# Kernel tuning notes

Hardware: AMD Instinct MI355X
Metric: run time of the kernel (lower is better)

## Reference

```python
import jax, jax.numpy as jnp
import numpy as np

N, E, C_IN, H, K = 16384, 524288, 128, 64, 64


def setup_inputs() -> dict:
    key = jax.random.key(0)
    ks = jax.random.split(key, 6)
    x = jax.random.normal(ks[0], (N, C_IN), dtype=jnp.float32)
    edge_index = jax.random.randint(ks[1], (2, E), 0, N, dtype=jnp.int32)
    edge_weight = jax.random.uniform(ks[2], (E,), dtype=jnp.float32)
    sc = lambda f: 1.0 / np.sqrt(f)
    # GCNConv lin (no bias inside lin; separate bias), Glorot-ish init
    W1 = jax.random.normal(ks[3], (C_IN, H), dtype=jnp.float32) * sc(C_IN)
    b1 = jnp.zeros((H,), jnp.float32)
    # DMoNPooling MLP: Linear(H,H) then Linear(H,K), no activation between (act=None)
    Wm1 = jax.random.normal(ks[4], (H, H), dtype=jnp.float32) * sc(H)
    bm1 = jnp.zeros((H,), jnp.float32)
    Wm2 = jax.random.normal(ks[5], (H, K), dtype=jnp.float32) * sc(H)
    bm2 = jnp.zeros((K,), jnp.float32)
    return dict(x=x, edge_index=edge_index, edge_weight=edge_weight,
                W1=W1, b1=b1, Wm1=Wm1, bm1=bm1, Wm2=Wm2, bm2=bm2)


def gcn_conv(x, edge_index, edge_weight, W, b, n):
    # GCNConv: add self-loops (weight 1), symmetric deg^-1/2 normalization,
    # aggregate messages from source (row) into target (col).
    row, col = edge_index[0], edge_index[1]
    loop = jnp.arange(n, dtype=edge_index.dtype)
    row = jnp.concatenate([row, loop])
    col = jnp.concatenate([col, loop])
    w = jnp.concatenate([edge_weight, jnp.ones((n,), edge_weight.dtype)])
    deg = jax.ops.segment_sum(w, col, num_segments=n)
    dis = jnp.where(deg > 0, jax.lax.rsqrt(deg), 0.0)
    norm = dis[row] * w * dis[col]
    xw = x @ W  # [N, H]
    out = jax.ops.segment_sum(xw[row] * norm[:, None], col, num_segments=n)
    return out + b


def dmon_pool(h, adj, Wm1, bm1, Wm2, bm2):
    # eval mode: dropout disabled
    s = jax.nn.softmax((h @ Wm1 + bm1) @ Wm2 + bm2, axis=-1)  # [N, K]
    k = s.shape[-1]
    out_adj = s.T @ (adj @ s)  # [K, K]

    # Spectral (modularity) loss; degrees = einsum('ijk->ik', adj) = column sums
    deg = adj.sum(axis=0)  # [N]
    m = deg.sum() / 2
    ca = s.T @ deg  # [K], equals degrees^T s as well (symmetric roles)
    normalizer = jnp.outer(ca, ca) / 2 / m
    spectral_loss = -jnp.trace(out_adj - normalizer) / 2 / m

    # Orthogonality loss
    ss = s.T @ s  # [K, K]
    ss_fro = jnp.sqrt(jnp.sum(ss * ss))
    i_fro = jnp.sqrt(jnp.float32(k))  # ||I_K||_F
    diff = ss / ss_fro - jnp.eye(k, dtype=ss.dtype) / i_fro
    ortho_loss = jnp.sqrt(jnp.sum(diff * diff))

    # Cluster size loss
    cluster_size = s.sum(axis=0)  # [K]
    cluster_loss = jnp.sqrt(jnp.sum(cluster_size * cluster_size)) / h.shape[0] * i_fro - 1.0

    return s, spectral_loss, ortho_loss, cluster_loss


def reference(x, edge_index, edge_weight, W1, b1, Wm1, bm1, Wm2, bm2):
    h = jax.nn.relu(gcn_conv(x, edge_index, edge_weight, W1, b1, N))
    # to_dense_adj(edge_index): dense [N, N], duplicate edges summed
    adj = jnp.zeros((N, N), h.dtype).at[edge_index[0], edge_index[1]].add(1.0)
    s, spec, ortho, clus = dmon_pool(h, adj, Wm1, bm1, Wm2, bm2)
    return s[None], spec + ortho + clus
```

## Files before the change

### kernel.cpp

```cpp
#include <hip/hip_runtime.h>
#include <hip/hip_bf16.h>

typedef float          f4  __attribute__((ext_vector_type(4)));
typedef unsigned short us4 __attribute__((ext_vector_type(4)));
typedef int            i2  __attribute__((ext_vector_type(2)));

template <typename T>
__device__ __forceinline__ T ntload(const T* p) { return __builtin_nontemporal_load(p); }

__device__ __forceinline__ unsigned short f2bf(float f) {
    unsigned u = __float_as_uint(f);
    return (unsigned short)((u + 0x7FFF + ((u >> 16) & 1)) >> 16);
}
__device__ __forceinline__ float bf2f(unsigned short h) {
    return __uint_as_float((unsigned)h << 16);
}

__global__ __launch_bounds__(256) void k_degxw(const int* __restrict__ ei,
                      const float* __restrict__ ew,
                      unsigned long long* __restrict__ deg_rep,
                      const float* __restrict__ x, const float* __restrict__ W1,
                      float* __restrict__ xw, unsigned short* __restrict__ xw16,
                      int N, int E) {
    __shared__ float w1l[128 * 64];
    __shared__ f4    xt[16][32];
    if (blockIdx.x < 2048) {
        int e = blockIdx.x * 256 + threadIdx.x;
        if (e < E) {
            int c = ntload(ei + E + e);
            float w = ntload(ew + e);
            unsigned q = (unsigned)__float2uint_rn(w * 16777216.f);
            unsigned long long p = (1ULL << 40) | (unsigned long long)q;
            atomicAdd(&deg_rep[(size_t)(blockIdx.x & 7) * N + c], p);
        }
        return;
    }
    int xbid = blockIdx.x - 2048;
    for (int t = threadIdx.x; t < 128 * 64; t += 256) w1l[t] = W1[t];
    int lane = threadIdx.x & 63;
    int wv   = threadIdx.x >> 6;
    for (int base = xbid * 16; base < N; base += 512 * 16) {
        __syncthreads();
        for (int t = threadIdx.x; t < 16 * 32; t += 256)
            ((f4*)xt)[t] = ntload((const f4*)x + (size_t)base * 32 + t);
        __syncthreads();
        int r0 = wv * 4;
        float a0 = 0.f, a1 = 0.f, a2 = 0.f, a3 = 0.f;
#pragma unroll
        for (int q = 0; q < 32; ++q) {
            f4 x0 = xt[r0][q], x1 = xt[r0 + 1][q], x2 = xt[r0 + 2][q], x3 = xt[r0 + 3][q];
            float wa = w1l[(4 * q + 0) * 64 + lane];
            float wb = w1l[(4 * q + 1) * 64 + lane];
            float wc = w1l[(4 * q + 2) * 64 + lane];
            float wd = w1l[(4 * q + 3) * 64 + lane];
            a0 = fmaf(x0.x, wa, a0); a0 = fmaf(x0.y, wb, a0); a0 = fmaf(x0.z, wc, a0); a0 = fmaf(x0.w, wd, a0);
            a1 = fmaf(x1.x, wa, a1); a1 = fmaf(x1.y, wb, a1); a1 = fmaf(x1.z, wc, a1); a1 = fmaf(x1.w, wd, a1);
            a2 = fmaf(x2.x, wa, a2); a2 = fmaf(x2.y, wb, a2); a2 = fmaf(x2.z, wc, a2); a2 = fmaf(x2.w, wd, a2);
            a3 = fmaf(x3.x, wa, a3); a3 = fmaf(x3.y, wb, a3); a3 = fmaf(x3.z, wc, a3); a3 = fmaf(x3.w, wd, a3);
        }
        int gr = base + r0;
        __builtin_nontemporal_store(a0, xw + (size_t)(gr + 0) * 64 + lane);
        __builtin_nontemporal_store(a1, xw + (size_t)(gr + 1) * 64 + lane);
        __builtin_nontemporal_store(a2, xw + (size_t)(gr + 2) * 64 + lane);
        __builtin_nontemporal_store(a3, xw + (size_t)(gr + 3) * 64 + lane);
        xw16[(size_t)(gr + 0) * 64 + lane] = f2bf(a0);
        xw16[(size_t)(gr + 1) * 64 + lane] = f2bf(a1);
        xw16[(size_t)(gr + 2) * 64 + lane] = f2bf(a2);
        xw16[(size_t)(gr + 3) * 64 + lane] = f2bf(a3);
    }
}

__global__ void k_red(const unsigned long long* __restrict__ deg_rep,
                      int* __restrict__ off_rep, int* __restrict__ cnt,
                      float* __restrict__ dis, int N) {
    int c = blockIdx.x * blockDim.x + threadIdx.x;
    if (c >= N) return;
    int run = 0;
    unsigned long long wsum = 0;
#pragma unroll
    for (int rep = 0; rep < 8; ++rep) {
        unsigned long long p = deg_rep[(size_t)rep * N + c];
        off_rep[(size_t)rep * N + c] = run;
        run += (int)(p >> 40);
        wsum += (p & ((1ULL << 40) - 1));
    }
    cnt[c] = run;
    dis[c] = rsqrtf((float)wsum * (1.f / 16777216.f) + 1.0f);
}

__global__ void k_scan(const int* __restrict__ cnt, int* __restrict__ offs, int N) {
    __shared__ int part[1024];
    int tid = threadIdx.x;
    int C = (N + 1023) / 1024;
    int base = tid * C;
    int loc[16];
    int sum = 0;
#pragma unroll
    for (int i = 0; i < 16; ++i) {
        if (i < C) {
            int idx = base + i;
            loc[i] = sum;
            sum += (idx < N) ? cnt[idx] : 0;
        }
    }
    part[tid] = sum;
    __syncthreads();
    for (int o = 1; o < 1024; o <<= 1) {
        int t = (tid >= o) ? part[tid - o] : 0;
        __syncthreads();
        part[tid] += t;
        __syncthreads();
    }
    int excl = part[tid] - sum;
#pragma unroll
    for (int i = 0; i < 16; ++i) {
        if (i < C) {
            int idx = base + i;
            if (idx < N) offs[idx] = excl + loc[i];
        }
    }
    if (tid == 1023) offs[N] = part[tid];
}

__global__ void k_bucket(const int* __restrict__ ei, const float* __restrict__ ew,
                         const float* __restrict__ dis, const int* __restrict__ offs,
                         const int* __restrict__ off_rep, int* __restrict__ cursor_rep,
                         i2* __restrict__ barr, int N, int E) {
    int e = blockIdx.x * blockDim.x + threadIdx.x;
    if (e < E) {
        int rep = blockIdx.x & 7;
        int r = ntload(ei + e), c = ntload(ei + E + e);
        float norm = dis[r] * ntload(ew + e) * dis[c];
        size_t rc = (size_t)rep * N + c;
        int pos = offs[c] + off_rep[rc] + atomicAdd(&cursor_rep[rc], 1);
        i2 rec; rec.x = r; rec.y = __float_as_int(norm);
        __builtin_nontemporal_store(rec, barr + pos);
    }
}

__global__ __launch_bounds__(256) void k_gather(const int* __restrict__ offs,
                         const i2* __restrict__ barr,
                         const float* __restrict__ xw, const unsigned short* __restrict__ xw16,
                         const float* __restrict__ dis,
                         const float* __restrict__ b1, float* __restrict__ h, int N) {
    int lane = threadIdx.x & 63;
    int sub = lane >> 4, q = lane & 15;
    int wid  = blockIdx.x * 4 + (threadIdx.x >> 6);
    int nw   = 4 * gridDim.x;
    const us4* xw16v = (const us4*)xw16;
    for (int cp = wid; cp < (N >> 1); cp += nw) {
        int c0 = 2 * cp, c1 = c0 + 1;
        int beg = ntload(offs + c0), mid = ntload(offs + c1), end = ntload(offs + c1 + 1);
        f4 A0 = {0.f, 0.f, 0.f, 0.f}, A1 = A0, B0 = A0, B1 = A0;
        for (int i = beg; i < end; i += 64) {
            int nloc = min(64, end - i);
            bool ok = (i + lane < end);
            i2 b = ok ? ntload(barr + i + lane) : (i2){0, 0};
            int   rv = b.x;
            float nv = __int_as_float(b.y);
            int jmax = (nloc + 3) >> 2;
            int j = 0;
            for (; j + 4 <= jmax; j += 4) {
                int e0 = 4 * j + sub;
                int g0 = i + e0;
                int   r0 = __shfl(rv, e0),      r1 = __shfl(rv, e0 + 4);
                int   r2 = __shfl(rv, e0 + 8),  r3 = __shfl(rv, e0 + 12);
                float n0 = __shfl(nv, e0),      n1 = __shfl(nv, e0 + 4);
                float n2 = __shfl(nv, e0 + 8),  n3 = __shfl(nv, e0 + 12);
                us4 u0 = xw16v[(size_t)r0 * 16 + q];
                us4 u1 = xw16v[(size_t)r1 * 16 + q];
                us4 u2 = xw16v[(size_t)r2 * 16 + q];
                us4 u3 = xw16v[(size_t)r3 * 16 + q];
                float a0w = (g0      < mid) ? n0 : 0.f, b0w = n0 - a0w;
                float a1w = (g0 + 4  < mid) ? n1 : 0.f, b1w = n1 - a1w;
                float a2w = (g0 + 8  < mid) ? n2 : 0.f, b2w = n2 - a2w;
                float a3w = (g0 + 12 < mid) ? n3 : 0.f, b3w = n3 - a3w;
                A0.x = fmaf(bf2f(u0.x), a0w, A0.x); A0.y = fmaf(bf2f(u0.y), a0w, A0.y);
                A0.z = fmaf(bf2f(u0.z), a0w, A0.z); A0.w = fmaf(bf2f(u0.w), a0w, A0.w);
                B0.x = fmaf(bf2f(u0.x), b0w, B0.x); B0.y = fmaf(bf2f(u0.y), b0w, B0.y);
                B0.z = fmaf(bf2f(u0.z), b0w, B0.z); B0.w = fmaf(bf2f(u0.w), b0w, B0.w);
                A1.x = fmaf(bf2f(u1.x), a1w, A1.x); A1.y = fmaf(bf2f(u1.y), a1w, A1.y);
                A1.z = fmaf(bf2f(u1.z), a1w, A1.z); A1.w = fmaf(bf2f(u1.w), a1w, A1.w);
                B1.x = fmaf(bf2f(u1.x), b1w, B1.x); B1.y = fmaf(bf2f(u1.y), b1w, B1.y);
                B1.z = fmaf(bf2f(u1.z), b1w, B1.z); B1.w = fmaf(bf2f(u1.w), b1w, B1.w);
                A0.x = fmaf(bf2f(u2.x), a2w, A0.x); A0.y = fmaf(bf2f(u2.y), a2w, A0.y);
                A0.z = fmaf(bf2f(u2.z), a2w, A0.z); A0.w = fmaf(bf2f(u2.w), a2w, A0.w);
                B0.x = fmaf(bf2f(u2.x), b2w, B0.x); B0.y = fmaf(bf2f(u2.y), b2w, B0.y);
                B0.z = fmaf(bf2f(u2.z), b2w, B0.z); B0.w = fmaf(bf2f(u2.w), b2w, B0.w);
                A1.x = fmaf(bf2f(u3.x), a3w, A1.x); A1.y = fmaf(bf2f(u3.y), a3w, A1.y);
                A1.z = fmaf(bf2f(u3.z), a3w, A1.z); A1.w = fmaf(bf2f(u3.w), a3w, A1.w);
                B1.x = fmaf(bf2f(u3.x), b3w, B1.x); B1.y = fmaf(bf2f(u3.y), b3w, B1.y);
                B1.z = fmaf(bf2f(u3.z), b3w, B1.z); B1.w = fmaf(bf2f(u3.w), b3w, B1.w);
            }
            for (; j < jmax; ++j) {
                int e = 4 * j + sub;
                int g = i + e;
                int   r  = __shfl(rv, e);
                float nm = __shfl(nv, e);
                us4 u = xw16v[(size_t)r * 16 + q];
                float aw = (g < mid) ? nm : 0.f, bw = nm - aw;
                A0.x = fmaf(bf2f(u.x), aw, A0.x); A0.y = fmaf(bf2f(u.y), aw, A0.y);
                A0.z = fmaf(bf2f(u.z), aw, A0.z); A0.w = fmaf(bf2f(u.w), aw, A0.w);
                B0.x = fmaf(bf2f(u.x), bw, B0.x); B0.y = fmaf(bf2f(u.y), bw, B0.y);
                B0.z = fmaf(bf2f(u.z), bw, B0.z); B0.w = fmaf(bf2f(u.w), bw, B0.w);
            }
        }
        A0.x += A1.x; A0.y += A1.y; A0.z += A1.z; A0.w += A1.w;
        B0.x += B1.x; B0.y += B1.y; B0.z += B1.z; B0.w += B1.w;
        A0.x += __shfl_xor(A0.x, 16); A0.y += __shfl_xor(A0.y, 16);
        A0.z += __shfl_xor(A0.z, 16); A0.w += __shfl_xor(A0.w, 16);
        B0.x += __shfl_xor(B0.x, 16); B0.y += __shfl_xor(B0.y, 16);
        B0.z += __shfl_xor(B0.z, 16); B0.w += __shfl_xor(B0.w, 16);
        A0.x += __shfl_xor(A0.x, 32); A0.y += __shfl_xor(A0.y, 32);
        A0.z += __shfl_xor(A0.z, 32); A0.w += __shfl_xor(A0.w, 32);
        B0.x += __shfl_xor(B0.x, 32); B0.y += __shfl_xor(B0.y, 32);
        B0.z += __shfl_xor(B0.z, 32); B0.w += __shfl_xor(B0.w, 32);
        f4 bb = ((const f4*)b1)[q];
        f4 self0 = ntload((const f4*)xw + (size_t)c0 * 16 + q);
        f4 self1 = ntload((const f4*)xw + (size_t)c1 * 16 + q);
        float d0 = dis[c0], d1 = dis[c1];
        float dd0 = d0 * d0, dd1 = d1 * d1;
        f4 v0, v1;
        v0.x = A0.x + self0.x * dd0 + bb.x; v0.y = A0.y + self0.y * dd0 + bb.y;
        v0.z = A0.z + self0.z * dd0 + bb.z; v0.w = A0.w + self0.w * dd0 + bb.w;
        v1.x = B0.x + self1.x * dd1 + bb.x; v1.y = B0.y + self1.y * dd1 + bb.y;
        v1.z = B0.z + self1.z * dd1 + bb.z; v1.w = B0.w + self1.w * dd1 + bb.w;
        v0.x = v0.x > 0.f ? v0.x : 0.f; v0.y = v0.y > 0.f ? v0.y : 0.f;
        v0.z = v0.z > 0.f ? v0.z : 0.f; v0.w = v0.w > 0.f ? v0.w : 0.f;
        v1.x = v1.x > 0.f ? v1.x : 0.f; v1.y = v1.y > 0.f ? v1.y : 0.f;
        v1.z = v1.z > 0.f ? v1.z : 0.f; v1.w = v1.w > 0.f ? v1.w : 0.f;
        if (sub == 0) {
            __builtin_nontemporal_store(v0, (f4*)h + (size_t)c0 * 16 + q);
            __builtin_nontemporal_store(v1, (f4*)h + (size_t)c1 * 16 + q);
        }
    }
}

__global__ __launch_bounds__(256) void k_mlp(const float* __restrict__ h,
                      const float* __restrict__ Wm1, const float* __restrict__ bm1,
                      const float* __restrict__ Wm2, const float* __restrict__ bm2,
                      float* __restrict__ s, unsigned short* __restrict__ s16, int N) {
    __shared__ float w1l[4096], w2l[4096], b1l[64], b2l[64];
    __shared__ f4    ht[16][16];
    __shared__ float tt[4][4][64];
    for (int t = threadIdx.x; t < 4096; t += 256) {
        w1l[t] = Wm1[t];
        w2l[t] = Wm2[t];
    }
    if (threadIdx.x < 64) {
        b1l[threadIdx.x] = bm1[threadIdx.x];
        b2l[threadIdx.x] = bm2[threadIdx.x];
    }
    int lane = threadIdx.x & 63;
    int wv   = threadIdx.x >> 6;
    for (int base = blockIdx.x * 16; base < N; base += gridDim.x * 16) {
        __syncthreads();
        for (int t = threadIdx.x; t < 16 * 16; t += 256)
            ((f4*)ht)[t] = ntload((const f4*)h + (size_t)base * 16 + t);
        __syncthreads();
        int r0 = wv * 4;
        float t0 = b1l[lane], t1 = t0, t2 = t0, t3 = t0;
#pragma unroll
        for (int q = 0; q < 16; ++q) {
            f4 h0 = ht[r0][q], h1 = ht[r0 + 1][q], h2 = ht[r0 + 2][q], h3 = ht[r0 + 3][q];
            float wa = w1l[(4 * q + 0) * 64 + lane];
            float wb = w1l[(4 * q + 1) * 64 + lane];
            float wc = w1l[(4 * q + 2) * 64 + lane];
            float wd = w1l[(4 * q + 3) * 64 + lane];
            t0 = fmaf(h0.x, wa, t0); t0 = fmaf(h0.y, wb, t0); t0 = fmaf(h0.z, wc, t0); t0 = fmaf(h0.w, wd, t0);
            t1 = fmaf(h1.x, wa, t1); t1 = fmaf(h1.y, wb, t1); t1 = fmaf(h1.z, wc, t1); t1 = fmaf(h1.w, wd, t1);
            t2 = fmaf(h2.x, wa, t2); t2 = fmaf(h2.y, wb, t2); t2 = fmaf(h2.z, wc, t2); t2 = fmaf(h2.w, wd, t2);
            t3 = fmaf(h3.x, wa, t3); t3 = fmaf(h3.y, wb, t3); t3 = fmaf(h3.z, wc, t3); t3 = fmaf(h3.w, wd, t3);
        }
        tt[wv][0][lane] = t0; tt[wv][1][lane] = t1;
        tt[wv][2][lane] = t2; tt[wv][3][lane] = t3;
        __syncthreads();
        float g0 = b2l[lane], g1 = g0, g2 = g0, g3 = g0;
#pragma unroll
        for (int q = 0; q < 16; ++q) {
            f4 u0 = ((f4*)tt[wv][0])[q], u1 = ((f4*)tt[wv][1])[q];
            f4 u2 = ((f4*)tt[wv][2])[q], u3 = ((f4*)tt[wv][3])[q];
            float wa = w2l[(4 * q + 0) * 64 + lane];
            float wb = w2l[(4 * q + 1) * 64 + lane];
            float wc = w2l[(4 * q + 2) * 64 + lane];
            float wd = w2l[(4 * q + 3) * 64 + lane];
            g0 = fmaf(u0.x, wa, g0); g0 = fmaf(u0.y, wb, g0); g0 = fmaf(u0.z, wc, g0); g0 = fmaf(u0.w, wd, g0);
            g1 = fmaf(u1.x, wa, g1); g1 = fmaf(u1.y, wb, g1); g1 = fmaf(u1.z, wc, g1); g1 = fmaf(u1.w, wd, g1);
            g2 = fmaf(u2.x, wa, g2); g2 = fmaf(u2.y, wb, g2); g2 = fmaf(u2.z, wc, g2); g2 = fmaf(u2.w, wd, g2);
            g3 = fmaf(u3.x, wa, g3); g3 = fmaf(u3.y, wb, g3); g3 = fmaf(u3.z, wc, g3); g3 = fmaf(u3.w, wd, g3);
        }
        float m0 = g0, m1 = g1, m2 = g2, m3 = g3;
#pragma unroll
        for (int o = 32; o > 0; o >>= 1) {
            m0 = fmaxf(m0, __shfl_xor(m0, o));
            m1 = fmaxf(m1, __shfl_xor(m1, o));
            m2 = fmaxf(m2, __shfl_xor(m2, o));
            m3 = fmaxf(m3, __shfl_xor(m3, o));
        }
        float e0 = __expf(g0 - m0), e1 = __expf(g1 - m1);
        float e2 = __expf(g2 - m2), e3 = __expf(g3 - m3);
        float s0 = e0, s1 = e1, s2 = e2, s3 = e3;
#pragma unroll
        for (int o = 32; o > 0; o >>= 1) {
            s0 += __shfl_xor(s0, o);
            s1 += __shfl_xor(s1, o);
            s2 += __shfl_xor(s2, o);
            s3 += __shfl_xor(s3, o);
        }
        int gr = base + r0;
        float o0 = e0 / s0, o1 = e1 / s1, o2 = e2 / s2, o3 = e3 / s3;
        __builtin_nontemporal_store(o0, s + (size_t)(gr + 0) * 64 + lane);
        __builtin_nontemporal_store(o1, s + (size_t)(gr + 1) * 64 + lane);
        __builtin_nontemporal_store(o2, s + (size_t)(gr + 2) * 64 + lane);
        __builtin_nontemporal_store(o3, s + (size_t)(gr + 3) * 64 + lane);
        s16[(size_t)(gr + 0) * 64 + lane] = f2bf(o0);
        s16[(size_t)(gr + 1) * 64 + lane] = f2bf(o1);
        s16[(size_t)(gr + 2) * 64 + lane] = f2bf(o2);
        s16[(size_t)(gr + 3) * 64 + lane] = f2bf(o3);
    }
}

__global__ __launch_bounds__(256) void k_rt(const int* __restrict__ offs,
                         const i2* __restrict__ barr,
                         const unsigned short* __restrict__ s16,
                         const float* __restrict__ s, const int* __restrict__ cnt,
                         float* __restrict__ ssg, float* __restrict__ cag,
                         float* __restrict__ csg, float* __restrict__ tracearr, int N) {
    __shared__ float tile[64][64];
    __shared__ float bsum;
    int lane = threadIdx.x & 63;
    int wv   = threadIdx.x >> 6;
    if (blockIdx.x >= 2048) {
        int base = (blockIdx.x - 2048) * 64;
        if (base >= N) return;
        for (int t = threadIdx.x; t < 1024; t += 256)
            ((f4*)tile)[t] = ntload((const f4*)(s + (size_t)base * 64) + t);
        __syncthreads();
        float acc[16];
#pragma unroll
        for (int i = 0; i < 16; ++i) acc[i] = 0.f;
        for (int r = 0; r < 64; ++r) {
            float sj = tile[r][lane];
            const float* brow = &tile[r][wv * 16];
#pragma unroll
            for (int i = 0; i < 16; ++i) acc[i] = fmaf(brow[i], sj, acc[i]);
        }
        float csj = 0.f, caj = 0.f;
#pragma unroll
        for (int i = 0; i < 16; ++i) {
            int r = wv * 16 + i;
            float sj = tile[r][lane];
            csj += sj;
            caj = fmaf(sj, (float)cnt[base + r], caj);
        }
#pragma unroll
        for (int i = 0; i < 16; ++i) atomicAdd(&ssg[(wv * 16 + i) * 64 + lane], acc[i]);
        atomicAdd(&csg[lane], csj);
        atomicAdd(&cag[lane], caj);
        return;
    }
    int sub = lane >> 4, q = lane & 15;
    int wid  = blockIdx.x * 4 + wv;
    int nw   = 4 * 2048;
    const us4* s16v = (const us4*)s16;
    float tacc = 0.f;
    for (int cp = wid; cp < (N >> 1); cp += nw) {
        int c0 = 2 * cp, c1 = c0 + 1;
        int beg = ntload(offs + c0), mid = ntload(offs + c1), end = ntload(offs + c1 + 1);
        us4 scu0 = s16v[(size_t)c0 * 16 + q];
        us4 scu1 = s16v[(size_t)c1 * 16 + q];
        f4 sc0 = {bf2f(scu0.x), bf2f(scu0.y), bf2f(scu0.z), bf2f(scu0.w)};
        f4 sc1 = {bf2f(scu1.x), bf2f(scu1.y), bf2f(scu1.z), bf2f(scu1.w)};
        f4 A0 = {0.f, 0.f, 0.f, 0.f}, A1 = A0, B0 = A0, B1 = A0;
        for (int i = beg; i < end; i += 64) {
            int nloc = min(64, end - i);
            int rv = (i + lane < end) ? ntload(barr + i + lane).x : 0;
            int jmax = (nloc + 3) >> 2;
            int j = 0;
            for (; j + 4 <= jmax; j += 4) {
                int e0 = 4 * j + sub;
                int g0 = i + e0;
                int r0 = __shfl(rv, e0),     r1 = __shfl(rv, e0 + 4);
                int r2 = __shfl(rv, e0 + 8), r3 = __shfl(rv, e0 + 12);
                float n0 = (e0      < nloc) ? 1.f : 0.f;
                float n1 = (e0 + 4  < nloc) ? 1.f : 0.f;
                float n2 = (e0 + 8  < nloc) ? 1.f : 0.f;
                float n3 = (e0 + 12 < nloc) ? 1.f : 0.f;
                us4 u0 = s16v[(size_t)r0 * 16 + q];
                us4 u1 = s16v[(size_t)r1 * 16 + q];
                us4 u2 = s16v[(size_t)r2 * 16 + q];
                us4 u3 = s16v[(size_t)r3 * 16 + q];
                float a0w = (g0      < mid) ? n0 : 0.f, b0w = n0 - a0w;
                float a1w = (g0 + 4  < mid) ? n1 : 0.f, b1w = n1 - a1w;
                float a2w = (g0 + 8  < mid) ? n2 : 0.f, b2w = n2 - a2w;
                float a3w = (g0 + 12 < mid) ? n3 : 0.f, b3w = n3 - a3w;
                A0.x = fmaf(bf2f(u0.x), a0w, A0.x); A0.y = fmaf(bf2f(u0.y), a0w, A0.y);
                A0.z = fmaf(bf2f(u0.z), a0w, A0.z); A0.w = fmaf(bf2f(u0.w), a0w, A0.w);
                B0.x = fmaf(bf2f(u0.x), b0w, B0.x); B0.y = fmaf(bf2f(u0.y), b0w, B0.y);
                B0.z = fmaf(bf2f(u0.z), b0w, B0.z); B0.w = fmaf(bf2f(u0.w), b0w, B0.w);
                A1.x = fmaf(bf2f(u1.x), a1w, A1.x); A1.y = fmaf(bf2f(u1.y), a1w, A1.y);
                A1.z = fmaf(bf2f(u1.z), a1w, A1.z); A1.w = fmaf(bf2f(u1.w), a1w, A1.w);
                B1.x = fmaf(bf2f(u1.x), b1w, B1.x); B1.y = fmaf(bf2f(u1.y), b1w, B1.y);
                B1.z = fmaf(bf2f(u1.z), b1w, B1.z); B1.w = fmaf(bf2f(u1.w), b1w, B1.w);
                A0.x = fmaf(bf2f(u2.x), a2w, A0.x); A0.y = fmaf(bf2f(u2.y), a2w, A0.y);
                A0.z = fmaf(bf2f(u2.z), a2w, A0.z); A0.w = fmaf(bf2f(u2.w), a2w, A0.w);
                B0.x = fmaf(bf2f(u2.x), b2w, B0.x); B0.y = fmaf(bf2f(u2.y), b2w, B0.y);
                B0.z = fmaf(bf2f(u2.z), b2w, B0.z); B0.w = fmaf(bf2f(u2.w), b2w, B0.w);
                A1.x = fmaf(bf2f(u3.x), a3w, A1.x); A1.y = fmaf(bf2f(u3.y), a3w, A1.y);
                A1.z = fmaf(bf2f(u3.z), a3w, A1.z); A1.w = fmaf(bf2f(u3.w), a3w, A1.w);
                B1.x = fmaf(bf2f(u3.x), b3w, B1.x); B1.y = fmaf(bf2f(u3.y), b3w, B1.y);
                B1.z = fmaf(bf2f(u3.z), b3w, B1.z); B1.w = fmaf(bf2f(u3.w), b3w, B1.w);
            }
            for (; j < jmax; ++j) {
                int e = 4 * j + sub;
                int g = i + e;
                int r = __shfl(rv, e);
                float m = (e < nloc) ? 1.f : 0.f;
                us4 u = s16v[(size_t)r * 16 + q];
                float aw = (g < mid) ? m : 0.f, bw = m - aw;
                A0.x = fmaf(bf2f(u.x), aw, A0.x); A0.y = fmaf(bf2f(u.y), aw, A0.y);
                A0.z = fmaf(bf2f(u.z), aw, A0.z); A0.w = fmaf(bf2f(u.w), aw, A0.w);
                B0.x = fmaf(bf2f(u.x), bw, B0.x); B0.y = fmaf(bf2f(u.y), bw, B0.y);
                B0.z = fmaf(bf2f(u.z), bw, B0.z); B0.w = fmaf(bf2f(u.w), bw, B0.w);
            }
        }
        A0.x += A1.x; A0.y += A1.y; A0.z += A1.z; A0.w += A1.w;
        B0.x += B1.x; B0.y += B1.y; B0.z += B1.z; B0.w += B1.w;
        A0.x += __shfl_xor(A0.x, 16); A0.y += __shfl_xor(A0.y, 16);
        A0.z += __shfl_xor(A0.z, 16); A0.w += __shfl_xor(A0.w, 16);
        B0.x += __shfl_xor(B0.x, 16); B0.y += __shfl_xor(B0.y, 16);
        B0.z += __shfl_xor(B0.z, 16); B0.w += __shfl_xor(B0.w, 16);
        A0.x += __shfl_xor(A0.x, 32); A0.y += __shfl_xor(A0.y, 32);
        A0.z += __shfl_xor(A0.z, 32); A0.w += __shfl_xor(A0.w, 32);
        B0.x += __shfl_xor(B0.x, 32); B0.y += __shfl_xor(B0.y, 32);
        B0.z += __shfl_xor(B0.z, 32); B0.w += __shfl_xor(B0.w, 32);
        tacc += A0.x * sc0.x + A0.y * sc0.y + A0.z * sc0.z + A0.w * sc0.w;
        tacc += B0.x * sc1.x + B0.y * sc1.y + B0.z * sc1.z + B0.w * sc1.w;
    }
    tacc *= 0.25f;
#pragma unroll
    for (int o = 32; o > 0; o >>= 1) tacc += __shfl_xor(tacc, o);
    if (threadIdx.x == 0) bsum = 0.f;
    __syncthreads();
    if (lane == 0) atomicAdd(&bsum, tacc);
    __syncthreads();
    if (threadIdx.x == 0) tracearr[blockIdx.x] = bsum;
}

__global__ void k_final(const float* __restrict__ ssg, const float* __restrict__ cag,
                        const float* __restrict__ csg, const float* __restrict__ tracearr,
                        int ntr, float Ef, float Nf, float* __restrict__ out) {
    __shared__ float red[256];
    int tid = threadIdx.x;

    float a = 0.f;
    for (int t = tid; t < ntr; t += 256) a += tracearr[t];
    red[tid] = a; __syncthreads();
    for (int o = 128; o > 0; o >>= 1) { if (tid < o) red[tid] += red[tid + o]; __syncthreads(); }
    float trace = red[0]; __syncthreads();

    a = 0.f;
    for (int t = tid; t < 4096; t += 256) { float v = ssg[t]; a += v * v; }
    red[tid] = a; __syncthreads();
    for (int o = 128; o > 0; o >>= 1) { if (tid < o) red[tid] += red[tid + o]; __syncthreads(); }
    float ss_sumsq = red[0]; __syncthreads();

    a = (tid < 64) ? ssg[tid * 64 + tid] : 0.f;
    red[tid] = a; __syncthreads();
    for (int o = 128; o > 0; o >>= 1) { if (tid < o) red[tid] += red[tid + o]; __syncthreads(); }
    float tr_ss = red[0]; __syncthreads();

    a = (tid < 64) ? cag[tid] * cag[tid] : 0.f;
    red[tid] = a; __syncthreads();
    for (int o = 128; o > 0; o >>= 1) { if (tid < o) red[tid] += red[tid + o]; __syncthreads(); }
    float ca_ss = red[0]; __syncthreads();

    a = (tid < 64) ? csg[tid] * csg[tid] : 0.f;
    red[tid] = a; __syncthreads();
    for (int o = 128; o > 0; o >>= 1) { if (tid < o) red[tid] += red[tid + o]; __syncthreads(); }
    float cs_ss = red[0];

    if (tid == 0) {
        float spec = -(trace - ca_ss / Ef) / Ef;
        float ss_fro = sqrtf(ss_sumsq);
        float ortho = sqrtf(fmaxf(2.f - tr_ss / (4.f * ss_fro), 0.f));
        float clus = sqrtf(cs_ss) / Nf * 8.f - 1.f;
        out[0] = spec + ortho + clus;
    }
}

extern "C" void kernel_launch(void* const* d_in, const int* in_sizes, int n_in,
                              void* d_out, int out_size, void* d_ws, size_t ws_size,
                              hipStream_t stream) {
    const float* x   = (const float*)d_in[0];
    const int*   ei  = (const int*)d_in[1];
    const float* ew  = (const float*)d_in[2];
    const float* W1  = (const float*)d_in[3];
    const float* b1  = (const float*)d_in[4];
    const float* Wm1 = (const float*)d_in[5];
    const float* bm1 = (const float*)d_in[6];
    const float* Wm2 = (const float*)d_in[7];
    const float* bm2 = (const float*)d_in[8];
    float* out = (float*)d_out;

    const int N = in_sizes[0] / 128;
    const int E = in_sizes[2];
    const int TGRID = 2304;

    char* base = (char*)d_ws;
    unsigned long long* deg_rep = (unsigned long long*)base;
    int*   cursor_rep = (int*)(base + (size_t)64 * N);
    float* ssg = (float*)(base + (size_t)96 * N);
    float* cag = ssg + 4096;
    float* csg = cag + 64;
    size_t zbytes = (size_t)96 * N + (4096 + 128) * 4;
    char* up = base + ((zbytes + 15) & ~(size_t)15);
    int*   cnt = (int*)up;            up += (size_t)4 * N;
    float* dis = (float*)up;          up += (size_t)4 * N;
    int*   offs = (int*)up;           up += (size_t)4 * (N + 1);
    float* tracearr = (float*)up;     up += (size_t)4 * TGRID;
    up = (char*)(((size_t)up + 15) & ~(size_t)15);
    float* xw = (float*)up;           up += (size_t)4 * N * 64;
    float* h  = (float*)up;           up += (size_t)4 * N * 64;
    int*   off_rep = (int*)h;
    i2*    barr = (i2*)up;            up += (size_t)8 * E;
    unsigned short* xw16 = (unsigned short*)up; up += (size_t)2 * N * 64;
    unsigned short* s16  = (unsigned short*)up;
    float* sbuf = out;

    hipMemsetAsync(d_ws, 0, zbytes, stream);

    k_degxw<<<2560, 256, 0, stream>>>(ei, ew, deg_rep, x, W1, xw, xw16, N, E);
    k_red<<<(N + 255) / 256, 256, 0, stream>>>(deg_rep, off_rep, cnt, dis, N);
    k_scan<<<1, 1024, 0, stream>>>(cnt, offs, N);
    k_bucket<<<(E + 255) / 256, 256, 0, stream>>>(ei, ew, dis, offs, off_rep, cursor_rep, barr, N, E);
    k_gather<<<2048, 256, 0, stream>>>(offs, barr, xw, xw16, dis, b1, h, N);
    k_mlp<<<512, 256, 0, stream>>>(h, Wm1, bm1, Wm2, bm2, sbuf, s16, N);
    k_rt<<<TGRID, 256, 0, stream>>>(offs, barr, s16, sbuf, cnt, ssg, cag, csg, tracearr, N);
    k_final<<<1, 256, 0, stream>>>(ssg, cag, csg, tracearr, TGRID, (float)E, (float)N,
                                   out + (size_t)N * 64);
}
```

Before: 233.7 us.

## Fuse GCN gather with MLP softmax and fold final loss reduction into last block

The gather kernel now runs the two-layer MLP and softmax directly on each wave's freshly aggregated node rows. Weights sit in shared memory and the h values are broadcast with shuffles, so the intermediate h buffer and its write and read round trip go away. The separate final loss kernel is merged into the trace kernel using a done counter, so the last block to finish computes the loss. This removes two launches and one full N×64 memory pass, at the cost of a larger 512-thread block with 32KB of shared weights that may reduce occupancy in the gather.

```diff
diff --git a/kernel.cpp b/kernel.cpp
--- a/kernel.cpp
+++ b/kernel.cpp
@@ -138,15 +138,22 @@
     }
 }
 
-__global__ __launch_bounds__(256) void k_gather(const int* __restrict__ offs,
+__global__ __launch_bounds__(512) void k_gmlp(const int* __restrict__ offs,
                          const i2* __restrict__ barr,
                          const float* __restrict__ xw, const unsigned short* __restrict__ xw16,
-                         const float* __restrict__ dis,
-                         const float* __restrict__ b1, float* __restrict__ h, int N) {
+                         const float* __restrict__ dis, const float* __restrict__ b1,
+                         const float* __restrict__ Wm1, const float* __restrict__ bm1,
+                         const float* __restrict__ Wm2, const float* __restrict__ bm2,
+                         float* __restrict__ s, unsigned short* __restrict__ s16, int N) {
+    __shared__ float w1m[4096], w2m[4096];
+    __shared__ float tsc[8][2][64];
+    for (int t = threadIdx.x; t < 4096; t += 512) { w1m[t] = Wm1[t]; w2m[t] = Wm2[t]; }
+    __syncthreads();
     int lane = threadIdx.x & 63;
     int sub = lane >> 4, q = lane & 15;
-    int wid  = blockIdx.x * 4 + (threadIdx.x >> 6);
-    int nw   = 4 * gridDim.x;
+    int wv   = threadIdx.x >> 6;
+    int wid  = blockIdx.x * 8 + wv;
+    int nw   = 8 * gridDim.x;
     const us4* xw16v = (const us4*)xw16;
     for (int cp = wid; cp < (N >> 1); cp += nw) {
         int c0 = 2 * cp, c1 = c0 + 1;
@@ -229,232 +236,195 @@
         v0.z = v0.z > 0.f ? v0.z : 0.f; v0.w = v0.w > 0.f ? v0.w : 0.f;
         v1.x = v1.x > 0.f ? v1.x : 0.f; v1.y = v1.y > 0.f ? v1.y : 0.f;
         v1.z = v1.z > 0.f ? v1.z : 0.f; v1.w = v1.w > 0.f ? v1.w : 0.f;
-        if (sub == 0) {
-            __builtin_nontemporal_store(v0, (f4*)h + (size_t)c0 * 16 + q);
-            __builtin_nontemporal_store(v1, (f4*)h + (size_t)c1 * 16 + q);
-        }
-    }
-}
-
-__global__ __launch_bounds__(256) void k_mlp(const float* __restrict__ h,
-                      const float* __restrict__ Wm1, const float* __restrict__ bm1,
-                      const float* __restrict__ Wm2, const float* __restrict__ bm2,
-                      float* __restrict__ s, unsigned short* __restrict__ s16, int N) {
-    __shared__ float w1l[4096], w2l[4096], b1l[64], b2l[64];
-    __shared__ f4    ht[16][16];
-    __shared__ float tt[4][4][64];
-    for (int t = threadIdx.x; t < 4096; t += 256) {
-        w1l[t] = Wm1[t];
-        w2l[t] = Wm2[t];
-    }
-    if (threadIdx.x < 64) {
-        b1l[threadIdx.x] = bm1[threadIdx.x];
-        b2l[threadIdx.x] = bm2[threadIdx.x];
-    }
-    int lane = threadIdx.x & 63;
-    int wv   = threadIdx.x >> 6;
-    for (int base = blockIdx.x * 16; base < N; base += gridDim.x * 16) {
-        __syncthreads();
-        for (int t = threadIdx.x; t < 16 * 16; t += 256)
-            ((f4*)ht)[t] = ntload((const f4*)h + (size_t)base * 16 + t);
-        __syncthreads();
-        int r0 = wv * 4;
-        float t0 = b1l[lane], t1 = t0, t2 = t0, t3 = t0;
-#pragma unroll
-        for (int q = 0; q < 16; ++q) {
-            f4 h0 = ht[r0][q], h1 = ht[r0 + 1][q], h2 = ht[r0 + 2][q], h3 = ht[r0 + 3][q];
-            float wa = w1l[(4 * q + 0) * 64 + lane];
-            float wb = w1l[(4 * q + 1) * 64 + lane];
-            float wc = w1l[(4 * q + 2) * 64 + lane];
-            float wd = w1l[(4 * q + 3) * 64 + lane];
-            t0 = fmaf(h0.x, wa, t0); t0 = fmaf(h0.y, wb, t0); t0 = fmaf(h0.z, wc, t0); t0 = fmaf(h0.w, wd, t0);
-            t1 = fmaf(h1.x, wa, t1); t1 = fmaf(h1.y, wb, t1); t1 = fmaf(h1.z, wc, t1); t1 = fmaf(h1.w, wd, t1);
-            t2 = fmaf(h2.x, wa, t2); t2 = fmaf(h2.y, wb, t2); t2 = fmaf(h2.z, wc, t2); t2 = fmaf(h2.w, wd, t2);
-            t3 = fmaf(h3.x, wa, t3); t3 = fmaf(h3.y, wb, t3); t3 = fmaf(h3.z, wc, t3); t3 = fmaf(h3.w, wd, t3);
-        }
-        tt[wv][0][lane] = t0; tt[wv][1][lane] = t1;
-        tt[wv][2][lane] = t2; tt[wv][3][lane] = t3;
-        __syncthreads();
-        float g0 = b2l[lane], g1 = g0, g2 = g0, g3 = g0;
-#pragma unroll
-        for (int q = 0; q < 16; ++q) {
-            f4 u0 = ((f4*)tt[wv][0])[q], u1 = ((f4*)tt[wv][1])[q];
-            f4 u2 = ((f4*)tt[wv][2])[q], u3 = ((f4*)tt[wv][3])[q];
-            float wa = w2l[(4 * q + 0) * 64 + lane];
-            float wb = w2l[(4 * q + 1) * 64 + lane];
-            float wc = w2l[(4 * q + 2) * 64 + lane];
-            float wd = w2l[(4 * q + 3) * 64 + lane];
-            g0 = fmaf(u0.x, wa, g0); g0 = fmaf(u0.y, wb, g0); g0 = fmaf(u0.z, wc, g0); g0 = fmaf(u0.w, wd, g0);
-            g1 = fmaf(u1.x, wa, g1); g1 = fmaf(u1.y, wb, g1); g1 = fmaf(u1.z, wc, g1); g1 = fmaf(u1.w, wd, g1);
-            g2 = fmaf(u2.x, wa, g2); g2 = fmaf(u2.y, wb, g2); g2 = fmaf(u2.z, wc, g2); g2 = fmaf(u2.w, wd, g2);
-            g3 = fmaf(u3.x, wa, g3); g3 = fmaf(u3.y, wb, g3); g3 = fmaf(u3.z, wc, g3); g3 = fmaf(u3.w, wd, g3);
-        }
-        float m0 = g0, m1 = g1, m2 = g2, m3 = g3;
+        float t0 = bm1[lane], t1 = t0;
+#pragma unroll
+        for (int k = 0; k < 16; ++k) {
+            float wa = w1m[(4 * k + 0) * 64 + lane];
+            float wb = w1m[(4 * k + 1) * 64 + lane];
+            float wc = w1m[(4 * k + 2) * 64 + lane];
+            float wd = w1m[(4 * k + 3) * 64 + lane];
+            t0 = fmaf(__shfl(v0.x, k), wa, t0); t0 = fmaf(__shfl(v0.y, k), wb, t0);
+            t0 = fmaf(__shfl(v0.z, k), wc, t0); t0 = fmaf(__shfl(v0.w, k), wd, t0);
+            t1 = fmaf(__shfl(v1.x, k), wa, t1); t1 = fmaf(__shfl(v1.y, k), wb, t1);
+            t1 = fmaf(__shfl(v1.z, k), wc, t1); t1 = fmaf(__shfl(v1.w, k), wd, t1);
+        }
+        tsc[wv][0][lane] = t0;
+        tsc[wv][1][lane] = t1;
+        float g0 = bm2[lane], g1 = g0;
+#pragma unroll
+        for (int k = 0; k < 16; ++k) {
+            f4 ta = ((f4*)tsc[wv][0])[k];
+            f4 tb = ((f4*)tsc[wv][1])[k];
+            float wa = w2m[(4 * k + 0) * 64 + lane];
+            float wb = w2m[(4 * k + 1) * 64 + lane];
+            float wc = w2m[(4 * k + 2) * 64 + lane];
+            float wd = w2m[(4 * k + 3) * 64 + lane];
+            g0 = fmaf(ta.x, wa, g0); g0 = fmaf(ta.y, wb, g0);
+            g0 = fmaf(ta.z, wc, g0); g0 = fmaf(ta.w, wd, g0);
+            g1 = fmaf(tb.x, wa, g1); g1 = fmaf(tb.y, wb, g1);
+            g1 = fmaf(tb.z, wc, g1); g1 = fmaf(tb.w, wd, g1);
+        }
+        float m0 = g0, m1 = g1;
 #pragma unroll
         for (int o = 32; o > 0; o >>= 1) {
             m0 = fmaxf(m0, __shfl_xor(m0, o));
             m1 = fmaxf(m1, __shfl_xor(m1, o));
-            m2 = fmaxf(m2, __shfl_xor(m2, o));
-            m3 = fmaxf(m3, __shfl_xor(m3, o));
         }
         float e0 = __expf(g0 - m0), e1 = __expf(g1 - m1);
-        float e2 = __expf(g2 - m2), e3 = __expf(g3 - m3);
-        float s0 = e0, s1 = e1, s2 = e2, s3 = e3;
+        float z0 = e0, z1 = e1;
 #pragma unroll
         for (int o = 32; o > 0; o >>= 1) {
-            s0 += __shfl_xor(s0, o);
-            s1 += __shfl_xor(s1, o);
-            s2 += __shfl_xor(s2, o);
-            s3 += __shfl_xor(s3, o);
-        }
-        int gr = base + r0;
-        float o0 = e0 / s0, o1 = e1 / s1, o2 = e2 / s2, o3 = e3 / s3;
-        __builtin_nontemporal_store(o0, s + (size_t)(gr + 0) * 64 + lane);
-        __builtin_nontemporal_store(o1, s + (size_t)(gr + 1) * 64 + lane);
-        __builtin_nontemporal_store(o2, s + (size_t)(gr + 2) * 64 + lane);
-        __builtin_nontemporal_store(o3, s + (size_t)(gr + 3) * 64 + lane);
-        s16[(size_t)(gr + 0) * 64 + lane] = f2bf(o0);
-        s16[(size_t)(gr + 1) * 64 + lane] = f2bf(o1);
-        s16[(size_t)(gr + 2) * 64 + lane] = f2bf(o2);
-        s16[(size_t)(gr + 3) * 64 + lane] = f2bf(o3);
-    }
-}
-
-__global__ __launch_bounds__(256) void k_rt(const int* __restrict__ offs,
+            z0 += __shfl_xor(z0, o);
+            z1 += __shfl_xor(z1, o);
+        }
+        float o0 = e0 / z0, o1 = e1 / z1;
+        __builtin_nontemporal_store(o0, s + (size_t)c0 * 64 + lane);
+        __builtin_nontemporal_store(o1, s + (size_t)c1 * 64 + lane);
+        s16[(size_t)c0 * 64 + lane] = f2bf(o0);
+        s16[(size_t)c1 * 64 + lane] = f2bf(o1);
+    }
+}
+
+__global__ __launch_bounds__(256) void k_rtfin(const int* __restrict__ offs,
                          const i2* __restrict__ barr,
                          const unsigned short* __restrict__ s16,
                          const float* __restrict__ s, const int* __restrict__ cnt,
                          float* __restrict__ ssg, float* __restrict__ cag,
-                         float* __restrict__ csg, float* __restrict__ tracearr, int N) {
+                         float* __restrict__ csg, float* __restrict__ tracearr,
+                         unsigned* __restrict__ done, float Ef, float Nf,
+                         float* __restrict__ loss, int N) {
     __shared__ float tile[64][64];
     __shared__ float bsum;
+    __shared__ unsigned tck;
     int lane = threadIdx.x & 63;
     int wv   = threadIdx.x >> 6;
     if (blockIdx.x >= 2048) {
         int base = (blockIdx.x - 2048) * 64;
-        if (base >= N) return;
-        for (int t = threadIdx.x; t < 1024; t += 256)
-            ((f4*)tile)[t] = ntload((const f4*)(s + (size_t)base * 64) + t);
+        if (base < N) {
+            for (int t = threadIdx.x; t < 1024; t += 256)
+                ((f4*)tile)[t] = ntload((const f4*)(s + (size_t)base * 64) + t);
+            __syncthreads();
+            float acc[16];
+#pragma unroll
+            for (int i = 0; i < 16; ++i) acc[i] = 0.f;
+            for (int r = 0; r < 64; ++r) {
+                float sj = tile[r][lane];
+                const float* brow = &tile[r][wv * 16];
+#pragma unroll
+                for (int i = 0; i < 16; ++i) acc[i] = fmaf(brow[i], sj, acc[i]);
+            }
+            float csj = 0.f, caj = 0.f;
+#pragma unroll
+            for (int i = 0; i < 16; ++i) {
+                int r = wv * 16 + i;
+                float sj = tile[r][lane];
+                csj += sj;
+                caj = fmaf(sj, (float)cnt[base + r], caj);
+            }
+#pragma unroll
+            for (int i = 0; i < 16; ++i) atomicAdd(&ssg[(wv * 16 + i) * 64 + lane], acc[i]);
+            atomicAdd(&csg[lane], csj);
+            atomicAdd(&cag[lane], caj);
+        }
+    } else {
+        int sub = lane >> 4, q = lane & 15;
+        int wid  = blockIdx.x * 4 + wv;
+        int nw   = 4 * 2048;
+        const us4* s16v = (const us4*)s16;
+        float tacc = 0.f;
+        for (int cp = wid; cp < (N >> 1); cp += nw) {
+            int c0 = 2 * cp, c1 = c0 + 1;
+            int beg = ntload(offs + c0), mid = ntload(offs + c1), end = ntload(offs + c1 + 1);
+            us4 scu0 = s16v[(size_t)c0 * 16 + q];
+            us4 scu1 = s16v[(size_t)c1 * 16 + q];
+            f4 sc0 = {bf2f(scu0.x), bf2f(scu0.y), bf2f(scu0.z), bf2f(scu0.w)};
+            f4 sc1 = {bf2f(scu1.x), bf2f(scu1.y), bf2f(scu1.z), bf2f(scu1.w)};
+            f4 A0 = {0.f, 0.f, 0.f, 0.f}, A1 = A0, B0 = A0, B1 = A0;
+            for (int i = beg; i < end; i += 64) {
+                int nloc = min(64, end - i);
+                int rv = (i + lane < end) ? ntload(barr + i + lane).x : 0;
+                int jmax = (nloc + 3) >> 2;
+                int j = 0;
+                for (; j + 4 <= jmax; j += 4) {
+                    int e0 = 4 * j + sub;
+                    int g0 = i + e0;
+                    int r0 = __shfl(rv, e0),     r1 = __shfl(rv, e0 + 4);
+                    int r2 = __shfl(rv, e0 + 8), r3 = __shfl(rv, e0 + 12);
+                    float n0 = (e0      < nloc) ? 1.f : 0.f;
+                    float n1 = (e0 + 4  < nloc) ? 1.f : 0.f;
+                    float n2 = (e0 + 8  < nloc) ? 1.f : 0.f;
+                    float n3 = (e0 + 12 < nloc) ? 1.f : 0.f;
+                    us4 u0 = s16v[(size_t)r0 * 16 + q];
+                    us4 u1 = s16v[(size_t)r1 * 16 + q];
+                    us4 u2 = s16v[(size_t)r2 * 16 + q];
+                    us4 u3 = s16v[(size_t)r3 * 16 + q];
+                    float a0w = (g0      < mid) ? n0 : 0.f, b0w = n0 - a0w;
+                    float a1w = (g0 + 4  < mid) ? n1 : 0.f, b1w = n1 - a1w;
+                    float a2w = (g0 + 8  < mid) ? n2 : 0.f, b2w = n2 - a2w;
+                    float a3w = (g0 + 12 < mid) ? n3 : 0.f, b3w = n3 - a3w;
+                    A0.x = fmaf(bf2f(u0.x), a0w, A0.x); A0.y = fmaf(bf2f(u0.y), a0w, A0.y);
+                    A0.z = fmaf(bf2f(u0.z), a0w, A0.z); A0.w = fmaf(bf2f(u0.w), a0w, A0.w);
+                    B0.x = fmaf(bf2f(u0.x), b0w, B0.x); B0.y = fmaf(bf2f(u0.y), b0w, B0.y);
+                    B0.z = fmaf(bf2f(u0.z), b0w, B0.z); B0.w = fmaf(bf2f(u0.w), b0w, B0.w);
+                    A1.x = fmaf(bf2f(u1.x), a1w, A1.x); A1.y = fmaf(bf2f(u1.y), a1w, A1.y);
+                    A1.z = fmaf(bf2f(u1.z), a1w, A1.z); A1.w = fmaf(bf2f(u1.w), a1w, A1.w);
+                    B1.x = fmaf(bf2f(u1.x), b1w, B1.x); B1.y = fmaf(bf2f(u1.y), b1w, B1.y);
+                    B1.z = fmaf(bf2f(u1.z), b1w, B1.z); B1.w = fmaf(bf2f(u1.w), b1w, B1.w);
+                    A0.x = fmaf(bf2f(u2.x), a2w, A0.x); A0.y = fmaf(bf2f(u2.y), a2w, A0.y);
+                    A0.z = fmaf(bf2f(u2.z), a2w, A0.z); A0.w = fmaf(bf2f(u2.w), a2w, A0.w);
+                    B0.x = fmaf(bf2f(u2.x), b2w, B0.x); B0.y = fmaf(bf2f(u2.y), b2w, B0.y);
+                    B0.z = fmaf(bf2f(u2.z), b2w, B0.z); B0.w = fmaf(bf2f(u2.w), b2w, B0.w);
+                    A1.x = fmaf(bf2f(u3.x), a3w, A1.x); A1.y = fmaf(bf2f(u3.y), a3w, A1.y);
+                    A1.z = fmaf(bf2f(u3.z), a3w, A1.z); A1.w = fmaf(bf2f(u3.w), a3w, A1.w);
+                    B1.x = fmaf(bf2f(u3.x), b3w, B1.x); B1.y = fmaf(bf2f(u3.y), b3w, B1.y);
+                    B1.z = fmaf(bf2f(u3.z), b3w, B1.z); B1.w = fmaf(bf2f(u3.w), b3w, B1.w);
+                }
+                for (; j < jmax; ++j) {
+                    int e = 4 * j + sub;
+                    int g = i + e;
+                    int r = __shfl(rv, e);
+                    float m = (e < nloc) ? 1.f : 0.f;
+                    us4 u = s16v[(size_t)r * 16 + q];
+                    float aw = (g < mid) ? m : 0.f, bw = m - aw;
+                    A0.x = fmaf(bf2f(u.x), aw, A0.x); A0.y = fmaf(bf2f(u.y), aw, A0.y);
+                    A0.z = fmaf(bf2f(u.z), aw, A0.z); A0.w = fmaf(bf2f(u.w), aw, A0.w);
+                    B0.x = fmaf(bf2f(u.x), bw, B0.x); B0.y = fmaf(bf2f(u.y), bw, B0.y);
+                    B0.z = fmaf(bf2f(u.z), bw, B0.z); B0.w = fmaf(bf2f(u.w), bw, B0.w);
+                }
+            }
+            A0.x += A1.x; A0.y += A1.y; A0.z += A1.z; A0.w += A1.w;
+            B0.x += B1.x; B0.y += B1.y; B0.z += B1.z; B0.w += B1.w;
+            A0.x += __shfl_xor(A0.x, 16); A0.y += __shfl_xor(A0.y, 16);
+            A0.z += __shfl_xor(A0.z, 16); A0.w += __shfl_xor(A0.w, 16);
+            B0.x += __shfl_xor(B0.x, 16); B0.y += __shfl_xor(B0.y, 16);
+            B0.z += __shfl_xor(B0.z, 16); B0.w += __shfl_xor(B0.w, 16);
+            A0.x += __shfl_xor(A0.x, 32); A0.y += __shfl_xor(A0.y, 32);
+            A0.z += __shfl_xor(A0.z, 32); A0.w += __shfl_xor(A0.w, 32);
+            B0.x += __shfl_xor(B0.x, 32); B0.y += __shfl_xor(B0.y, 32);
+            B0.z += __shfl_xor(B0.z, 32); B0.w += __shfl_xor(B0.w, 32);
+            tacc += A0.x * sc0.x + A0.y * sc0.y + A0.z * sc0.z + A0.w * sc0.w;
+            tacc += B0.x * sc1.x + B0.y * sc1.y + B0.z * sc1.z + B0.w * sc1.w;
+        }
+        tacc *= 0.25f;
+#pragma unroll
+        for (int o = 32; o > 0; o >>= 1) tacc += __shfl_xor(tacc, o);
+        if (threadIdx.x == 0) bsum = 0.f;
         __syncthreads();
-        float acc[16];
-#pragma unroll
-        for (int i = 0; i < 16; ++i) acc[i] = 0.f;
-        for (int r = 0; r < 64; ++r) {
-            float sj = tile[r][lane];
-            const float* brow = &tile[r][wv * 16];
-#pragma unroll
-            for (int i = 0; i < 16; ++i) acc[i] = fmaf(brow[i], sj, acc[i]);
-        }
-        float csj = 0.f, caj = 0.f;
-#pragma unroll
-        for (int i = 0; i < 16; ++i) {
-            int r = wv * 16 + i;
-            float sj = tile[r][lane];
-            csj += sj;
-            caj = fmaf(sj, (float)cnt[base + r], caj);
-        }
-#pragma unroll
-        for (int i = 0; i < 16; ++i) atomicAdd(&ssg[(wv * 16 + i) * 64 + lane], acc[i]);
-        atomicAdd(&csg[lane], csj);
-        atomicAdd(&cag[lane], caj);
-        return;
-    }
-    int sub = lane >> 4, q = lane & 15;
-    int wid  = blockIdx.x * 4 + wv;
-    int nw   = 4 * 2048;
-    const us4* s16v = (const us4*)s16;
-    float tacc = 0.f;
-    for (int cp = wid; cp < (N >> 1); cp += nw) {
-        int c0 = 2 * cp, c1 = c0 + 1;
-        int beg = ntload(offs + c0), mid = ntload(offs + c1), end = ntload(offs + c1 + 1);
-        us4 scu0 = s16v[(size_t)c0 * 16 + q];
-        us4 scu1 = s16v[(size_t)c1 * 16 + q];
-        f4 sc0 = {bf2f(scu0.x), bf2f(scu0.y), bf2f(scu0.z), bf2f(scu0.w)};
-        f4 sc1 = {bf2f(scu1.x), bf2f(scu1.y), bf2f(scu1.z), bf2f(scu1.w)};
-        f4 A0 = {0.f, 0.f, 0.f, 0.f}, A1 = A0, B0 = A0, B1 = A0;
-        for (int i = beg; i < end; i += 64) {
-            int nloc = min(64, end - i);
-            int rv = (i + lane < end) ? ntload(barr + i + lane).x : 0;
-            int jmax = (nloc + 3) >> 2;
-            int j = 0;
-            for (; j + 4 <= jmax; j += 4) {
-                int e0 = 4 * j + sub;
-                int g0 = i + e0;
-                int r0 = __shfl(rv, e0),     r1 = __shfl(rv, e0 + 4);
-                int r2 = __shfl(rv, e0 + 8), r3 = __shfl(rv, e0 + 12);
-                float n0 = (e0      < nloc) ? 1.f : 0.f;
-                float n1 = (e0 + 4  < nloc) ? 1.f : 0.f;
-                float n2 = (e0 + 8  < nloc) ? 1.f : 0.f;
-                float n3 = (e0 + 12 < nloc) ? 1.f : 0.f;
-                us4 u0 = s16v[(size_t)r0 * 16 + q];
-                us4 u1 = s16v[(size_t)r1 * 16 + q];
-                us4 u2 = s16v[(size_t)r2 * 16 + q];
-                us4 u3 = s16v[(size_t)r3 * 16 + q];
-                float a0w = (g0      < mid) ? n0 : 0.f, b0w = n0 - a0w;
-                float a1w = (g0 + 4  < mid) ? n1 : 0.f, b1w = n1 - a1w;
-                float a2w = (g0 + 8  < mid) ? n2 : 0.f, b2w = n2 - a2w;
-                float a3w = (g0 + 12 < mid) ? n3 : 0.f, b3w = n3 - a3w;
-                A0.x = fmaf(bf2f(u0.x), a0w, A0.x); A0.y = fmaf(bf2f(u0.y), a0w, A0.y);
-                A0.z = fmaf(bf2f(u0.z), a0w, A0.z); A0.w = fmaf(bf2f(u0.w), a0w, A0.w);
-                B0.x = fmaf(bf2f(u0.x), b0w, B0.x); B0.y = fmaf(bf2f(u0.y), b0w, B0.y);
-                B0.z = fmaf(bf2f(u0.z), b0w, B0.z); B0.w = fmaf(bf2f(u0.w), b0w, B0.w);
-                A1.x = fmaf(bf2f(u1.x), a1w, A1.x); A1.y = fmaf(bf2f(u1.y), a1w, A1.y);
-                A1.z = fmaf(bf2f(u1.z), a1w, A1.z); A1.w = fmaf(bf2f(u1.w), a1w, A1.w);
-                B1.x = fmaf(bf2f(u1.x), b1w, B1.x); B1.y = fmaf(bf2f(u1.y), b1w, B1.y);
-                B1.z = fmaf(bf2f(u1.z), b1w, B1.z); B1.w = fmaf(bf2f(u1.w), b1w, B1.w);
-                A0.x = fmaf(bf2f(u2.x), a2w, A0.x); A0.y = fmaf(bf2f(u2.y), a2w, A0.y);
-                A0.z = fmaf(bf2f(u2.z), a2w, A0.z); A0.w = fmaf(bf2f(u2.w), a2w, A0.w);
-                B0.x = fmaf(bf2f(u2.x), b2w, B0.x); B0.y = fmaf(bf2f(u2.y), b2w, B0.y);
-                B0.z = fmaf(bf2f(u2.z), b2w, B0.z); B0.w = fmaf(bf2f(u2.w), b2w, B0.w);
-                A1.x = fmaf(bf2f(u3.x), a3w, A1.x); A1.y = fmaf(bf2f(u3.y), a3w, A1.y);
-                A1.z = fmaf(bf2f(u3.z), a3w, A1.z); A1.w = fmaf(bf2f(u3.w), a3w, A1.w);
-                B1.x = fmaf(bf2f(u3.x), b3w, B1.x); B1.y = fmaf(bf2f(u3.y), b3w, B1.y);
-                B1.z = fmaf(bf2f(u3.z), b3w, B1.z); B1.w = fmaf(bf2f(u3.w), b3w, B1.w);
-            }
-            for (; j < jmax; ++j) {
-                int e = 4 * j + sub;
-                int g = i + e;
-                int r = __shfl(rv, e);
-                float m = (e < nloc) ? 1.f : 0.f;
-                us4 u = s16v[(size_t)r * 16 + q];
-                float aw = (g < mid) ? m : 0.f, bw = m - aw;
-                A0.x = fmaf(bf2f(u.x), aw, A0.x); A0.y = fmaf(bf2f(u.y), aw, A0.y);
-                A0.z = fmaf(bf2f(u.z), aw, A0.z); A0.w = fmaf(bf2f(u.w), aw, A0.w);
-                B0.x = fmaf(bf2f(u.x), bw, B0.x); B0.y = fmaf(bf2f(u.y), bw, B0.y);
-                B0.z = fmaf(bf2f(u.z), bw, B0.z); B0.w = fmaf(bf2f(u.w), bw, B0.w);
-            }
-        }
-        A0.x += A1.x; A0.y += A1.y; A0.z += A1.z; A0.w += A1.w;
-        B0.x += B1.x; B0.y += B1.y; B0.z += B1.z; B0.w += B1.w;
-        A0.x += __shfl_xor(A0.x, 16); A0.y += __shfl_xor(A0.y, 16);
-        A0.z += __shfl_xor(A0.z, 16); A0.w += __shfl_xor(A0.w, 16);
-        B0.x += __shfl_xor(B0.x, 16); B0.y += __shfl_xor(B0.y, 16);
-        B0.z += __shfl_xor(B0.z, 16); B0.w += __shfl_xor(B0.w, 16);
-        A0.x += __shfl_xor(A0.x, 32); A0.y += __shfl_xor(A0.y, 32);
-        A0.z += __shfl_xor(A0.z, 32); A0.w += __shfl_xor(A0.w, 32);
-        B0.x += __shfl_xor(B0.x, 32); B0.y += __shfl_xor(B0.y, 32);
-        B0.z += __shfl_xor(B0.z, 32); B0.w += __shfl_xor(B0.w, 32);
-        tacc += A0.x * sc0.x + A0.y * sc0.y + A0.z * sc0.z + A0.w * sc0.w;
-        tacc += B0.x * sc1.x + B0.y * sc1.y + B0.z * sc1.z + B0.w * sc1.w;
-    }
-    tacc *= 0.25f;
-#pragma unroll
-    for (int o = 32; o > 0; o >>= 1) tacc += __shfl_xor(tacc, o);
-    if (threadIdx.x == 0) bsum = 0.f;
+        if (lane == 0) atomicAdd(&bsum, tacc);
+        __syncthreads();
+        if (threadIdx.x == 0) tracearr[blockIdx.x] = bsum;
+    }
     __syncthreads();
-    if (lane == 0) atomicAdd(&bsum, tacc);
+    __threadfence();
+    if (threadIdx.x == 0) tck = atomicAdd(done, 1u);
     __syncthreads();
-    if (threadIdx.x == 0) tracearr[blockIdx.x] = bsum;
-}
-
-__global__ void k_final(const float* __restrict__ ssg, const float* __restrict__ cag,
-                        const float* __restrict__ csg, const float* __restrict__ tracearr,
-                        int ntr, float Ef, float Nf, float* __restrict__ out) {
-    __shared__ float red[256];
+    if (tck != gridDim.x - 1u) return;
+    __threadfence();
+    float* red = &tile[0][0];
     int tid = threadIdx.x;
 
     float a = 0.f;
-    for (int t = tid; t < ntr; t += 256) a += tracearr[t];
+    for (int t = tid; t < 2048; t += 256) a += tracearr[t];
     red[tid] = a; __syncthreads();
     for (int o = 128; o > 0; o >>= 1) { if (tid < o) red[tid] += red[tid + o]; __syncthreads(); }
     float trace = red[0]; __syncthreads();
@@ -485,7 +455,7 @@
         float ss_fro = sqrtf(ss_sumsq);
         float ortho = sqrtf(fmaxf(2.f - tr_ss / (4.f * ss_fro), 0.f));
         float clus = sqrtf(cs_ss) / Nf * 8.f - 1.f;
-        out[0] = spec + ortho + clus;
+        loss[0] = spec + ortho + clus;
     }
 }
 
@@ -501,7 +471,6 @@
     const float* bm1 = (const float*)d_in[6];
     const float* Wm2 = (const float*)d_in[7];
     const float* bm2 = (const float*)d_in[8];
-    float* out = (float*)d_out;
 
     const int N = in_sizes[0] / 128;
     const int E = in_sizes[2];
@@ -513,20 +482,20 @@
     float* ssg = (float*)(base + (size_t)96 * N);
     float* cag = ssg + 4096;
     float* csg = cag + 64;
-    size_t zbytes = (size_t)96 * N + (4096 + 128) * 4;
+    unsigned* done_cnt = (unsigned*)(csg + 64);
+    size_t zbytes = (size_t)96 * N + (4096 + 128 + 4) * 4;
     char* up = base + ((zbytes + 15) & ~(size_t)15);
     int*   cnt = (int*)up;            up += (size_t)4 * N;
     float* dis = (float*)up;          up += (size_t)4 * N;
     int*   offs = (int*)up;           up += (size_t)4 * (N + 1);
-    float* tracearr = (float*)up;     up += (size_t)4 * TGRID;
+    float* tracearr = (float*)up;     up += (size_t)4 * 2048;
     up = (char*)(((size_t)up + 15) & ~(size_t)15);
     float* xw = (float*)up;           up += (size_t)4 * N * 64;
-    float* h  = (float*)up;           up += (size_t)4 * N * 64;
-    int*   off_rep = (int*)h;
+    int*   off_rep = (int*)up;        up += (size_t)32 * N;
     i2*    barr = (i2*)up;            up += (size_t)8 * E;
     unsigned short* xw16 = (unsigned short*)up; up += (size_t)2 * N * 64;
     unsigned short* s16  = (unsigned short*)up;
-    float* sbuf = out;
+    float* sbuf = (float*)d_out;
 
     hipMemsetAsync(d_ws, 0, zbytes, stream);
 
@@ -534,9 +503,8 @@
     k_red<<<(N + 255) / 256, 256, 0, stream>>>(deg_rep, off_rep, cnt, dis, N);
     k_scan<<<1, 1024, 0, stream>>>(cnt, offs, N);
     k_bucket<<<(E + 255) / 256, 256, 0, stream>>>(ei, ew, dis, offs, off_rep, cursor_rep, barr, N, E);
-    k_gather<<<2048, 256, 0, stream>>>(offs, barr, xw, xw16, dis, b1, h, N);
-    k_mlp<<<512, 256, 0, stream>>>(h, Wm1, bm1, Wm2, bm2, sbuf, s16, N);
-    k_rt<<<TGRID, 256, 0, stream>>>(offs, barr, s16, sbuf, cnt, ssg, cag, csg, tracearr, N);
-    k_final<<<1, 256, 0, stream>>>(ssg, cag, csg, tracearr, TGRID, (float)E, (float)N,
-                                   out + (size_t)N * 64);
-}
+    k_gmlp<<<1024, 512, 0, stream>>>(offs, barr, xw, xw16, dis, b1, Wm1, bm1, Wm2, bm2, sbuf, s16, N);
+    k_rtfin<<<TGRID, 256, 0, stream>>>(offs, barr, s16, sbuf, cnt, ssg, cag, csg, tracearr,
+                                       done_cnt, (float)E, (float)N,
+                                       ((float*)d_out) + (size_t)N * 64, N);
+}
```

Result: slower. 383.6 us (+64.1%).
